# Performance work log

Hardware: AMD Instinct MI355X
Metric: run time of the kernel (lower is better)

The kernel has to match this reference:

```python
import jax, jax.numpy as jnp
import numpy as np

N = 100000   # nodes
E = 1600000  # edges (avg in-degree 16)
D = 128      # feature dim (in_feats == out_feats)


def setup_inputs() -> dict:
    key = jax.random.key(0)
    ks = jax.random.split(key, 8)
    h = jax.random.normal(ks[0], (N, D), dtype=jnp.float32)
    src = jax.random.randint(ks[1], (E,), 0, N)
    dst = jax.random.randint(ks[2], (E,), 0, N)
    # Xavier-uniform linear weights (gain ~ relu per reset_parameters)
    gain = float(np.sqrt(2.0))
    bound = gain * float(np.sqrt(6.0 / (D + D)))
    def w(k):
        return jax.random.uniform(k, (D, D), jnp.float32, -bound, bound)
    return {
        "h": h, "src": src, "dst": dst,
        "W_self0": w(ks[3]), "b_self0": jnp.zeros((D,), jnp.float32), "W_neigh0": w(ks[4]),
        "W_self1": w(ks[5]), "b_self1": jnp.zeros((D,), jnp.float32), "W_neigh1": w(ks[6]),
    }


def _sage_mean(x, src, dst, W_self, b_self, W_neigh):
    """DGL SAGEConv('mean') with in_feats == out_feats (lin_before_mp False):
    neigh = mean_{(u->v) in E} x[u]; out = fc_self(x) + fc_neigh(neigh)."""
    msg = x[src]  # [E, D] gather along edges
    ssum = jax.ops.segment_sum(msg, dst, num_segments=N)          # [N, D]
    deg = jax.ops.segment_sum(jnp.ones((src.shape[0],), x.dtype), dst, num_segments=N)
    neigh = jnp.where(deg[:, None] > 0, ssum / jnp.maximum(deg, 1.0)[:, None], 0.0)
    return x @ W_self.T + b_self + neigh @ W_neigh.T


def reference(h, src, dst, W_self0, b_self0, W_neigh0, W_self1, b_self1, W_neigh1):
    # SAGENet.forward (eval mode: no DropEdge, no feat dropout)
    t1 = _sage_mean(h, src, dst, W_self0, b_self0, W_neigh0)
    t2 = _sage_mean(t1, src, dst, W_self1, b_self1, W_neigh1)
    # res = sum over outs = [h, t1/1, t2/2]
    return h + t1 + t2 * 0.5
```

## Files before the change

### kernel.cpp

```cpp
#include <hip/hip_runtime.h>

#define D 128
#define NPC 128
#define NBUCKC 782
#define BCAPC 2560
#define NPB 32
#define BCAP 768
#define BIN_THREADS 512
#define BIN_CHUNK 8192

typedef __bf16 bf16x8 __attribute__((ext_vector_type(8)));
typedef __bf16 bf16x4 __attribute__((ext_vector_type(4)));
typedef float f32x4 __attribute__((ext_vector_type(4)));
typedef float f32x2 __attribute__((ext_vector_type(2)));

__global__ void k_wfrag(const float* __restrict__ A, const float* __restrict__ B,
                        const float* __restrict__ C2, const float* __restrict__ Dp,
                        __bf16* __restrict__ o) {
    int t = blockIdx.x * 256 + threadIdx.x;
    int m = t >> 11, r = t & 2047;
    int kb = r >> 9, nf = (r >> 6) & 7, l = r & 63;
    int lr = l & 15, lg = l >> 4;
    const float* W = (m == 0) ? A : (m == 1) ? B : (m == 2) ? C2 : Dp;
    const float* p = W + (nf * 16 + lr) * D + kb * 32 + lg * 8;
    bf16x8 v;
#pragma unroll
    for (int j = 0; j < 8; ++j) v[j] = (__bf16)p[j];
    *(bf16x8*)(o + (size_t)t * 8) = v;
}

__global__ void k_hconv(const float* __restrict__ x, __bf16* __restrict__ obf,
                        uint2* __restrict__ of8, int n8) {
    int i = blockIdx.x * 256 + threadIdx.x;
    if (i >= n8) return;
    const float4* x4 = (const float4*)x;
    float4 u = x4[(size_t)i * 2];
    float4 v = x4[(size_t)i * 2 + 1];
    bf16x8 r;
    r[0] = (__bf16)u.x; r[1] = (__bf16)u.y; r[2] = (__bf16)u.z; r[3] = (__bf16)u.w;
    r[4] = (__bf16)v.x; r[5] = (__bf16)v.y; r[6] = (__bf16)v.z; r[7] = (__bf16)v.w;
    *(bf16x8*)(obf + (size_t)i * 8) = r;
    int w0 = __builtin_amdgcn_cvt_pk_fp8_f32(u.x, u.y, 0, false);
    w0 = __builtin_amdgcn_cvt_pk_fp8_f32(u.z, u.w, w0, true);
    int w1 = __builtin_amdgcn_cvt_pk_fp8_f32(v.x, v.y, 0, false);
    w1 = __builtin_amdgcn_cvt_pk_fp8_f32(v.z, v.w, w1, true);
    of8[i] = make_uint2((unsigned)w0, (unsigned)w1);
}

__global__ void k_cvt8(const __bf16* __restrict__ x, uint2* __restrict__ of8, int n8) {
    int i = blockIdx.x * 256 + threadIdx.x;
    if (i >= n8) return;
    bf16x8 v = *(const bf16x8*)(x + (size_t)i * 8);
    int w0 = __builtin_amdgcn_cvt_pk_fp8_f32((float)v[0], (float)v[1], 0, false);
    w0 = __builtin_amdgcn_cvt_pk_fp8_f32((float)v[2], (float)v[3], w0, true);
    int w1 = __builtin_amdgcn_cvt_pk_fp8_f32((float)v[4], (float)v[5], 0, false);
    w1 = __builtin_amdgcn_cvt_pk_fp8_f32((float)v[6], (float)v[7], w1, true);
    of8[i] = make_uint2((unsigned)w0, (unsigned)w1);
}

__global__ __launch_bounds__(BIN_THREADS) void k_bin(
    const int* __restrict__ src, const int* __restrict__ dst,
    int* __restrict__ bcnt, unsigned int* __restrict__ bbuf, int E) {
    __shared__ int hist[NBUCKC];
    __shared__ int rbase[NBUCKC];
    __shared__ int lcur[NBUCKC];
    int tid = threadIdx.x;
    int e0 = blockIdx.x * BIN_CHUNK;
    int e1 = min(e0 + BIN_CHUNK, E);
    for (int i = tid; i < NBUCKC; i += BIN_THREADS) hist[i] = 0;
    __syncthreads();
    for (int i = e0 + tid; i < e1; i += BIN_THREADS)
        atomicAdd(&hist[dst[i] >> 7], 1);
    __syncthreads();
    for (int i = tid; i < NBUCKC; i += BIN_THREADS) {
        int c = hist[i];
        rbase[i] = (c > 0) ? atomicAdd(&bcnt[i], c) : 0;
        lcur[i] = 0;
    }
    __syncthreads();
    for (int i = e0 + tid; i < e1; i += BIN_THREADS) {
        int d = dst[i];
        int b = d >> 7;
        int pos = rbase[b] + atomicAdd(&lcur[b], 1);
        if (pos < BCAPC)
            bbuf[(size_t)b * BCAPC + pos] =
                ((unsigned)(d & 127) << 17) | (unsigned)src[i];
    }
}

__global__ __launch_bounds__(256) void k_bagg(
    const uint2* __restrict__ X8,
    const unsigned int* __restrict__ bbuf, const int* __restrict__ bcnt,
    __bf16* __restrict__ NEI, int n) {
    __shared__ int lnbr[BCAP];
    __shared__ int ldeg[NPB];
    __shared__ int lrow[NPB];
    __shared__ int lcur[NPB];
    int b = blockIdx.x;
    int tid = threadIdx.x;
    int cb = b >> 2;
    int sub = b & 3;
    int base = b * NPB;
    int nb = min(NPB, n - base);
    int cnt = min(bcnt[cb], BCAPC);
    const unsigned int* bb = bbuf + (size_t)cb * BCAPC;

    if (tid < NPB) { ldeg[tid] = 0; lcur[tid] = 0; }
    __syncthreads();
    for (int i = tid; i < cnt; i += 256) {
        int ld7 = (int)(bb[i] >> 17);
        if ((ld7 >> 5) == sub) atomicAdd(&ldeg[ld7 & 31], 1);
    }
    __syncthreads();
    if (tid < NPB) lrow[tid] = ldeg[tid];
    __syncthreads();
    for (int off = 1; off < NPB; off <<= 1) {
        int v = 0;
        if (tid < NPB && tid >= off) v = lrow[tid - off];
        __syncthreads();
        if (tid < NPB) lrow[tid] += v;
        __syncthreads();
    }
    for (int i = tid; i < cnt; i += 256) {
        unsigned e = bb[i];
        int ld7 = (int)(e >> 17);
        if ((ld7 >> 5) != sub) continue;
        int ld = ld7 & 31;
        int pos = (lrow[ld] - ldeg[ld]) + atomicAdd(&lcur[ld], 1);
        if (pos < BCAP) lnbr[pos] = (int)(e & 0x1FFFF);
    }
    __syncthreads();

    int slot = tid >> 4;
    int c = tid & 15;
#define DEC_ACC(w)                                                        \
    {                                                                     \
        f32x2 p0 = __builtin_amdgcn_cvt_pk_f32_fp8((w).x, false);         \
        f32x2 p1 = __builtin_amdgcn_cvt_pk_f32_fp8((w).x, true);          \
        f32x2 p2 = __builtin_amdgcn_cvt_pk_f32_fp8((w).y, false);         \
        f32x2 p3 = __builtin_amdgcn_cvt_pk_f32_fp8((w).y, true);          \
        a[0] += p0[0]; a[1] += p0[1]; a[2] += p1[0]; a[3] += p1[1];       \
        a[4] += p2[0]; a[5] += p2[1]; a[6] += p3[0]; a[7] += p3[1];       \
    }
#pragma unroll
    for (int it = 0; it < NPB / 16; ++it) {
        int node = it * 16 + slot;
        if (node >= nb) break;
        int dv = ldeg[node];
        int beg = lrow[node] - dv;
        float a[8];
#pragma unroll
        for (int j = 0; j < 8; ++j) a[j] = 0.f;
        int i = 0;
        for (; i + 7 < dv; i += 8) {
            uint2 w0 = X8[(size_t)lnbr[beg + i + 0] * 16 + c];
            uint2 w1 = X8[(size_t)lnbr[beg + i + 1] * 16 + c];
            uint2 w2 = X8[(size_t)lnbr[beg + i + 2] * 16 + c];
            uint2 w3 = X8[(size_t)lnbr[beg + i + 3] * 16 + c];
            uint2 w4 = X8[(size_t)lnbr[beg + i + 4] * 16 + c];
            uint2 w5 = X8[(size_t)lnbr[beg + i + 5] * 16 + c];
            uint2 w6 = X8[(size_t)lnbr[beg + i + 6] * 16 + c];
            uint2 w7 = X8[(size_t)lnbr[beg + i + 7] * 16 + c];
            DEC_ACC(w0) DEC_ACC(w1) DEC_ACC(w2) DEC_ACC(w3)
            DEC_ACC(w4) DEC_ACC(w5) DEC_ACC(w6) DEC_ACC(w7)
        }
        for (; i + 3 < dv; i += 4) {
            uint2 w0 = X8[(size_t)lnbr[beg + i + 0] * 16 + c];
            uint2 w1 = X8[(size_t)lnbr[beg + i + 1] * 16 + c];
            uint2 w2 = X8[(size_t)lnbr[beg + i + 2] * 16 + c];
            uint2 w3 = X8[(size_t)lnbr[beg + i + 3] * 16 + c];
            DEC_ACC(w0) DEC_ACC(w1) DEC_ACC(w2) DEC_ACC(w3)
        }
        for (; i < dv; ++i) {
            uint2 w0 = X8[(size_t)lnbr[beg + i] * 16 + c];
            DEC_ACC(w0)
        }
        float s = dv > 0 ? 1.0f / (float)dv : 0.0f;
        bf16x8 r;
#pragma unroll
        for (int j = 0; j < 8; ++j) r[j] = (__bf16)(a[j] * s);
        *(bf16x8*)(NEI + (size_t)(base + node) * D + c * 8) = r;
    }
#undef DEC_ACC
}

__global__ __launch_bounds__(256, 3) void k_gemm2(
    const __bf16* __restrict__ Xb, const __bf16* __restrict__ NEIb,
    const __bf16* __restrict__ Wfs, const __bf16* __restrict__ Wfn,
    const float* __restrict__ bs, const float* __restrict__ H,
    __bf16* __restrict__ t1out, float* __restrict__ out, int n, int final_mode) {
    __shared__ __bf16 wls[16384];

    int tid = threadIdx.x;
    int wave = tid >> 6;
    int lane = tid & 63;
    int lr = lane & 15;
    int lg = lane >> 4;
    int rowbase = blockIdx.x * 128 + wave * 32;

    bf16x8 xf[2][4];
#pragma unroll
    for (int mf = 0; mf < 2; ++mf) {
        int r = rowbase + mf * 16 + lr;
#pragma unroll
        for (int kb = 0; kb < 4; ++kb) {
            bf16x8 a = (bf16x8)(__bf16)0.f;
            if (r < n) a = *(const bf16x8*)(Xb + (size_t)r * D + kb * 32 + lg * 8);
            xf[mf][kb] = a;
        }
    }

    f32x4 acc[2][8];
#pragma unroll
    for (int mf = 0; mf < 2; ++mf)
#pragma unroll
        for (int nf = 0; nf < 8; ++nf) acc[mf][nf] = (f32x4)(0.f);

    {
        const bf16x8* s = (const bf16x8*)Wfs;
#pragma unroll
        for (int i = 0; i < 8; ++i) {
            bf16x8 v = s[i * 256 + tid];
            *(bf16x8*)(wls + (size_t)(i * 256 + tid) * 8) = v;
        }
    }
    __syncthreads();
#pragma unroll
    for (int kb = 0; kb < 4; ++kb) {
#pragma unroll
        for (int nf = 0; nf < 8; ++nf) {
            bf16x8 bfr = *(const bf16x8*)(wls + (size_t)((kb * 8 + nf) * 64 + lane) * 8);
            acc[0][nf] = __builtin_amdgcn_mfma_f32_16x16x32_bf16(xf[0][kb], bfr, acc[0][nf], 0, 0, 0);
            acc[1][nf] = __builtin_amdgcn_mfma_f32_16x16x32_bf16(xf[1][kb], bfr, acc[1][nf], 0, 0, 0);
        }
    }

    bf16x8 nfr[2][4];
#pragma unroll
    for (int mf = 0; mf < 2; ++mf) {
        int r = rowbase + mf * 16 + lr;
#pragma unroll
        for (int kb = 0; kb < 4; ++kb) {
            bf16x8 a = (bf16x8)(__bf16)0.f;
            if (r < n) a = *(const bf16x8*)(NEIb + (size_t)r * D + kb * 32 + lg * 8);
            nfr[mf][kb] = a;
        }
    }
    __syncthreads();
    {
        const bf16x8* s = (const bf16x8*)Wfn;
#pragma unroll
        for (int i = 0; i < 8; ++i) {
            bf16x8 v = s[i * 256 + tid];
            *(bf16x8*)(wls + (size_t)(i * 256 + tid) * 8) = v;
        }
    }
    __syncthreads();
#pragma unroll
    for (int kb = 0; kb < 4; ++kb) {
#pragma unroll
        for (int nf = 0; nf < 8; ++nf) {
            bf16x8 bfr = *(const bf16x8*)(wls + (size_t)((kb * 8 + nf) * 64 + lane) * 8);
            acc[0][nf] = __builtin_amdgcn_mfma_f32_16x16x32_bf16(nfr[0][kb], bfr, acc[0][nf], 0, 0, 0);
            acc[1][nf] = __builtin_amdgcn_mfma_f32_16x16x32_bf16(nfr[1][kb], bfr, acc[1][nf], 0, 0, 0);
        }
    }

#pragma unroll
    for (int mf = 0; mf < 2; ++mf) {
#pragma unroll
        for (int q = 0; q < 4; ++q) {
            int r = rowbase + mf * 16 + lg * 4 + q;
            if (r >= n) continue;
            if (final_mode) {
                const __bf16* t1p = Xb + (size_t)r * D;
#pragma unroll
                for (int nf = 0; nf < 8; ++nf) {
                    int j = nf * 16 + lr;
                    out[(size_t)r * D + j] =
                        H[(size_t)r * D + j] + (float)t1p[j] + 0.5f * (acc[mf][nf][q] + bs[j]);
                }
            } else {
                __bf16* dp = t1out + (size_t)r * D;
#pragma unroll
                for (int nf = 0; nf < 8; ++nf) {
                    int j = nf * 16 + lr;
                    dp[j] = (__bf16)(acc[mf][nf][q] + bs[j]);
                }
            }
        }
    }
}

extern "C" void kernel_launch(void* const* d_in, const int* in_sizes, int n_in,
                              void* d_out, int out_size, void* d_ws, size_t ws_size,
                              hipStream_t stream) {
    const float* h = (const float*)d_in[0];
    const int* src = (const int*)d_in[1];
    const int* dst = (const int*)d_in[2];
    const float* Ws0 = (const float*)d_in[3];
    const float* b0 = (const float*)d_in[4];
    const float* Wn0 = (const float*)d_in[5];
    const float* Ws1 = (const float*)d_in[6];
    const float* b1 = (const float*)d_in[7];
    const float* Wn1 = (const float*)d_in[8];
    float* out = (float*)d_out;

    int N = in_sizes[0] / D;
    int E = in_sizes[1];

    char* ws = (char*)d_ws;
    __bf16* hbf = (__bf16*)ws;   ws += (size_t)N * D * sizeof(__bf16);
    __bf16* t1b = (__bf16*)ws;   ws += (size_t)N * D * sizeof(__bf16);
    unsigned int* bbuf = (unsigned int*)ws; ws += (size_t)NBUCKC * BCAPC * sizeof(unsigned int);
    int* bcnt = (int*)ws;        ws += (size_t)NBUCKC * sizeof(int);
    __bf16* Wf = (__bf16*)ws;    ws += (size_t)4 * 2048 * 8 * sizeof(__bf16);
    __bf16* NEI1 = (__bf16*)d_out;
    uint2* F8 = (uint2*)((char*)d_out + ((size_t)32 << 20));
    __bf16* NEI2 = hbf;

    hipMemsetAsync(bcnt, 0, (size_t)NBUCKC * sizeof(int), stream);

    int n8 = N * D / 8;
    k_wfrag<<<32, 256, 0, stream>>>(Ws0, Wn0, Ws1, Wn1, Wf);
    k_hconv<<<(n8 + 255) / 256, 256, 0, stream>>>(h, hbf, F8, n8);
    k_bin<<<(E + BIN_CHUNK - 1) / BIN_CHUNK, BIN_THREADS, 0, stream>>>(src, dst, bcnt, bbuf, E);

    int gb = (N + 127) / 128;
    int ab = (N + NPB - 1) / NPB;
    k_bagg<<<ab, 256, 0, stream>>>(F8, bbuf, bcnt, NEI1, N);
    k_gemm2<<<gb, 256, 0, stream>>>(hbf, NEI1, Wf + 0 * 16384, Wf + 1 * 16384,
                                    b0, nullptr, t1b, nullptr, N, 0);
    k_cvt8<<<(n8 + 255) / 256, 256, 0, stream>>>(t1b, F8, n8);
    k_bagg<<<ab, 256, 0, stream>>>(F8, bbuf, bcnt, NEI2, N);
    k_gemm2<<<gb, 256, 0, stream>>>(t1b, NEI2, Wf + 2 * 16384, Wf + 3 * 16384,
                                    b1, h, nullptr, out, N, 1);
}
```

Before: 189.5 us.

## Fuse neighbor aggregation with dense GEMM into one per-layer kernel

Merges the aggregation kernel and the GEMM kernel into a single k_layer kernel. Mean-aggregated neighbor features stay in shared memory, and each 32-node block runs the self and neighbor MFMAs directly instead of writing and re-reading an NEI buffer. The layer-1 epilogue also writes the FP8 copy of t1, which removes the separate bf16 copy of h and the k_cvt8 pass. The cost is a smaller GEMM tile per block, loading the full weight matrices into LDS once per 32 rows instead of once per 128, and higher LDS use per block that may lower occupancy. It also drops the node-count bound check and leaves a dead load loop in the code.

```diff
diff --git a/kernel.cpp b/kernel.cpp
--- a/kernel.cpp
+++ b/kernel.cpp
@@ -1,16 +1,15 @@
 #include <hip/hip_runtime.h>
 
 #define D 128
-#define NPC 128
 #define NBUCKC 782
 #define BCAPC 2560
 #define NPB 32
 #define BCAP 768
 #define BIN_THREADS 512
 #define BIN_CHUNK 8192
+#define NEIW 140
 
 typedef __bf16 bf16x8 __attribute__((ext_vector_type(8)));
-typedef __bf16 bf16x4 __attribute__((ext_vector_type(4)));
 typedef float f32x4 __attribute__((ext_vector_type(4)));
 typedef float f32x2 __attribute__((ext_vector_type(2)));
 
@@ -29,32 +28,16 @@
     *(bf16x8*)(o + (size_t)t * 8) = v;
 }
 
-__global__ void k_hconv(const float* __restrict__ x, __bf16* __restrict__ obf,
-                        uint2* __restrict__ of8, int n8) {
+__global__ void k_hconv8(const float* __restrict__ x, uint2* __restrict__ of8, int n8) {
     int i = blockIdx.x * 256 + threadIdx.x;
     if (i >= n8) return;
     const float4* x4 = (const float4*)x;
     float4 u = x4[(size_t)i * 2];
     float4 v = x4[(size_t)i * 2 + 1];
-    bf16x8 r;
-    r[0] = (__bf16)u.x; r[1] = (__bf16)u.y; r[2] = (__bf16)u.z; r[3] = (__bf16)u.w;
-    r[4] = (__bf16)v.x; r[5] = (__bf16)v.y; r[6] = (__bf16)v.z; r[7] = (__bf16)v.w;
-    *(bf16x8*)(obf + (size_t)i * 8) = r;
     int w0 = __builtin_amdgcn_cvt_pk_fp8_f32(u.x, u.y, 0, false);
     w0 = __builtin_amdgcn_cvt_pk_fp8_f32(u.z, u.w, w0, true);
     int w1 = __builtin_amdgcn_cvt_pk_fp8_f32(v.x, v.y, 0, false);
     w1 = __builtin_amdgcn_cvt_pk_fp8_f32(v.z, v.w, w1, true);
-    of8[i] = make_uint2((unsigned)w0, (unsigned)w1);
-}
-
-__global__ void k_cvt8(const __bf16* __restrict__ x, uint2* __restrict__ of8, int n8) {
-    int i = blockIdx.x * 256 + threadIdx.x;
-    if (i >= n8) return;
-    bf16x8 v = *(const bf16x8*)(x + (size_t)i * 8);
-    int w0 = __builtin_amdgcn_cvt_pk_fp8_f32((float)v[0], (float)v[1], 0, false);
-    w0 = __builtin_amdgcn_cvt_pk_fp8_f32((float)v[2], (float)v[3], w0, true);
-    int w1 = __builtin_amdgcn_cvt_pk_fp8_f32((float)v[4], (float)v[5], 0, false);
-    w1 = __builtin_amdgcn_cvt_pk_fp8_f32((float)v[6], (float)v[7], w1, true);
     of8[i] = make_uint2((unsigned)w0, (unsigned)w1);
 }
 
@@ -88,22 +71,62 @@
     }
 }
 
-__global__ __launch_bounds__(256) void k_bagg(
+__global__ __launch_bounds__(256) void k_layer(
+    const float* __restrict__ Hf, const __bf16* __restrict__ T1,
     const uint2* __restrict__ X8,
     const unsigned int* __restrict__ bbuf, const int* __restrict__ bcnt,
-    __bf16* __restrict__ NEI, int n) {
+    const __bf16* __restrict__ Wfs, const __bf16* __restrict__ Wfn,
+    const float* __restrict__ bs,
+    __bf16* __restrict__ t1out, unsigned char* __restrict__ f8out,
+    float* __restrict__ out, int n, int final_mode) {
     __shared__ int lnbr[BCAP];
     __shared__ int ldeg[NPB];
     __shared__ int lrow[NPB];
     __shared__ int lcur[NPB];
+    __shared__ __bf16 nei[NPB * NEIW];
+    __shared__ __bf16 wls[16384];
+
     int b = blockIdx.x;
     int tid = threadIdx.x;
     int cb = b >> 2;
     int sub = b & 3;
     int base = b * NPB;
-    int nb = min(NPB, n - base);
     int cnt = min(bcnt[cb], BCAPC);
     const unsigned int* bb = bbuf + (size_t)cb * BCAPC;
+
+    int wave = tid >> 6;
+    int lane = tid & 63;
+    int lr = lane & 15;
+    int lg = lane >> 4;
+    int mf = wave & 1;
+    int nfh = wave >> 1;
+
+    bf16x8 xf[4];
+    {
+        int r = base + mf * 16 + lr;
+        if (final_mode) {
+#pragma unroll
+            for (int kb = 0; kb < 4; ++kb)
+                xf[kb] = *(const bf16x8*)(T1 + (size_t)r * D + kb * 32 + lg * 8);
+        } else {
+            const float4* p = (const float4*)(Hf + (size_t)r * D);
+#pragma unroll
+            for (int kb = 0; kb < 4; ++kb) {
+                float4 u = p[kb * 2 + (lg >> 1) * ((lg & 1) * 0)];
+                (void)u;
+            }
+#pragma unroll
+            for (int kb = 0; kb < 4; ++kb) {
+                const float4* q = (const float4*)(Hf + (size_t)r * D + kb * 32 + lg * 8);
+                float4 u = q[0];
+                float4 v = q[1];
+                bf16x8 a;
+                a[0] = (__bf16)u.x; a[1] = (__bf16)u.y; a[2] = (__bf16)u.z; a[3] = (__bf16)u.w;
+                a[4] = (__bf16)v.x; a[5] = (__bf16)v.y; a[6] = (__bf16)v.z; a[7] = (__bf16)v.w;
+                xf[kb] = a;
+            }
+        }
+    }
 
     if (tid < NPB) { ldeg[tid] = 0; lcur[tid] = 0; }
     __syncthreads();
@@ -131,26 +154,30 @@
     }
     __syncthreads();
 
+    {
+        const bf16x8* s = (const bf16x8*)Wfs;
+#pragma unroll
+        for (int i = 0; i < 8; ++i) {
+            bf16x8 v = s[i * 256 + tid];
+            *(bf16x8*)(wls + (size_t)(i * 256 + tid) * 8) = v;
+        }
+    }
+
     int slot = tid >> 4;
     int c = tid & 15;
 #define DEC_ACC(w)                                                        \
     {                                                                     \
-        f32x2 p0 = __builtin_amdgcn_cvt_pk_f32_fp8((w).x, false);         \
-        f32x2 p1 = __builtin_amdgcn_cvt_pk_f32_fp8((w).x, true);          \
-        f32x2 p2 = __builtin_amdgcn_cvt_pk_f32_fp8((w).y, false);         \
-        f32x2 p3 = __builtin_amdgcn_cvt_pk_f32_fp8((w).y, true);          \
-        a[0] += p0[0]; a[1] += p0[1]; a[2] += p1[0]; a[3] += p1[1];       \
-        a[4] += p2[0]; a[5] += p2[1]; a[6] += p3[0]; a[7] += p3[1];       \
+        a0 += __builtin_amdgcn_cvt_pk_f32_fp8((w).x, false);              \
+        a1 += __builtin_amdgcn_cvt_pk_f32_fp8((w).x, true);               \
+        a2 += __builtin_amdgcn_cvt_pk_f32_fp8((w).y, false);              \
+        a3 += __builtin_amdgcn_cvt_pk_f32_fp8((w).y, true);               \
     }
 #pragma unroll
     for (int it = 0; it < NPB / 16; ++it) {
         int node = it * 16 + slot;
-        if (node >= nb) break;
         int dv = ldeg[node];
         int beg = lrow[node] - dv;
-        float a[8];
-#pragma unroll
-        for (int j = 0; j < 8; ++j) a[j] = 0.f;
+        f32x2 a0 = (f32x2)(0.f), a1 = (f32x2)(0.f), a2 = (f32x2)(0.f), a3 = (f32x2)(0.f);
         int i = 0;
         for (; i + 7 < dv; i += 8) {
             uint2 w0 = X8[(size_t)lnbr[beg + i + 0] * 16 + c];
@@ -177,47 +204,30 @@
         }
         float s = dv > 0 ? 1.0f / (float)dv : 0.0f;
         bf16x8 r;
-#pragma unroll
-        for (int j = 0; j < 8; ++j) r[j] = (__bf16)(a[j] * s);
-        *(bf16x8*)(NEI + (size_t)(base + node) * D + c * 8) = r;
+        r[0] = (__bf16)(a0[0] * s); r[1] = (__bf16)(a0[1] * s);
+        r[2] = (__bf16)(a1[0] * s); r[3] = (__bf16)(a1[1] * s);
+        r[4] = (__bf16)(a2[0] * s); r[5] = (__bf16)(a2[1] * s);
+        r[6] = (__bf16)(a3[0] * s); r[7] = (__bf16)(a3[1] * s);
+        *(bf16x8*)(nei + node * NEIW + c * 8) = r;
     }
 #undef DEC_ACC
-}
-
-__global__ __launch_bounds__(256, 3) void k_gemm2(
-    const __bf16* __restrict__ Xb, const __bf16* __restrict__ NEIb,
-    const __bf16* __restrict__ Wfs, const __bf16* __restrict__ Wfn,
-    const float* __restrict__ bs, const float* __restrict__ H,
-    __bf16* __restrict__ t1out, float* __restrict__ out, int n, int final_mode) {
-    __shared__ __bf16 wls[16384];
-
-    int tid = threadIdx.x;
-    int wave = tid >> 6;
-    int lane = tid & 63;
-    int lr = lane & 15;
-    int lg = lane >> 4;
-    int rowbase = blockIdx.x * 128 + wave * 32;
-
-    bf16x8 xf[2][4];
-#pragma unroll
-    for (int mf = 0; mf < 2; ++mf) {
-        int r = rowbase + mf * 16 + lr;
-#pragma unroll
-        for (int kb = 0; kb < 4; ++kb) {
-            bf16x8 a = (bf16x8)(__bf16)0.f;
-            if (r < n) a = *(const bf16x8*)(Xb + (size_t)r * D + kb * 32 + lg * 8);
-            xf[mf][kb] = a;
-        }
-    }
-
-    f32x4 acc[2][8];
-#pragma unroll
-    for (int mf = 0; mf < 2; ++mf)
-#pragma unroll
-        for (int nf = 0; nf < 8; ++nf) acc[mf][nf] = (f32x4)(0.f);
-
+    __syncthreads();
+
+    f32x4 acc[4];
+#pragma unroll
+    for (int nfl = 0; nfl < 4; ++nfl) acc[nfl] = (f32x4)(0.f);
+#pragma unroll
+    for (int kb = 0; kb < 4; ++kb) {
+#pragma unroll
+        for (int nfl = 0; nfl < 4; ++nfl) {
+            int nf = nfh * 4 + nfl;
+            bf16x8 bfr = *(const bf16x8*)(wls + (size_t)((kb * 8 + nf) * 64 + lane) * 8);
+            acc[nfl] = __builtin_amdgcn_mfma_f32_16x16x32_bf16(xf[kb], bfr, acc[nfl], 0, 0, 0);
+        }
+    }
+    __syncthreads();
     {
-        const bf16x8* s = (const bf16x8*)Wfs;
+        const bf16x8* s = (const bf16x8*)Wfn;
 #pragma unroll
         for (int i = 0; i < 8; ++i) {
             bf16x8 v = s[i * 256 + tid];
@@ -227,66 +237,36 @@
     __syncthreads();
 #pragma unroll
     for (int kb = 0; kb < 4; ++kb) {
-#pragma unroll
-        for (int nf = 0; nf < 8; ++nf) {
+        bf16x8 af = *(const bf16x8*)(nei + (mf * 16 + lr) * NEIW + kb * 32 + lg * 8);
+#pragma unroll
+        for (int nfl = 0; nfl < 4; ++nfl) {
+            int nf = nfh * 4 + nfl;
             bf16x8 bfr = *(const bf16x8*)(wls + (size_t)((kb * 8 + nf) * 64 + lane) * 8);
-            acc[0][nf] = __builtin_amdgcn_mfma_f32_16x16x32_bf16(xf[0][kb], bfr, acc[0][nf], 0, 0, 0);
-            acc[1][nf] = __builtin_amdgcn_mfma_f32_16x16x32_bf16(xf[1][kb], bfr, acc[1][nf], 0, 0, 0);
-        }
-    }
-
-    bf16x8 nfr[2][4];
-#pragma unroll
-    for (int mf = 0; mf < 2; ++mf) {
-        int r = rowbase + mf * 16 + lr;
-#pragma unroll
-        for (int kb = 0; kb < 4; ++kb) {
-            bf16x8 a = (bf16x8)(__bf16)0.f;
-            if (r < n) a = *(const bf16x8*)(NEIb + (size_t)r * D + kb * 32 + lg * 8);
-            nfr[mf][kb] = a;
-        }
-    }
-    __syncthreads();
-    {
-        const bf16x8* s = (const bf16x8*)Wfn;
-#pragma unroll
-        for (int i = 0; i < 8; ++i) {
-            bf16x8 v = s[i * 256 + tid];
-            *(bf16x8*)(wls + (size_t)(i * 256 + tid) * 8) = v;
-        }
-    }
-    __syncthreads();
-#pragma unroll
-    for (int kb = 0; kb < 4; ++kb) {
-#pragma unroll
-        for (int nf = 0; nf < 8; ++nf) {
-            bf16x8 bfr = *(const bf16x8*)(wls + (size_t)((kb * 8 + nf) * 64 + lane) * 8);
-            acc[0][nf] = __builtin_amdgcn_mfma_f32_16x16x32_bf16(nfr[0][kb], bfr, acc[0][nf], 0, 0, 0);
-            acc[1][nf] = __builtin_amdgcn_mfma_f32_16x16x32_bf16(nfr[1][kb], bfr, acc[1][nf], 0, 0, 0);
-        }
-    }
-
-#pragma unroll
-    for (int mf = 0; mf < 2; ++mf) {
-#pragma unroll
-        for (int q = 0; q < 4; ++q) {
-            int r = rowbase + mf * 16 + lg * 4 + q;
-            if (r >= n) continue;
-            if (final_mode) {
-                const __bf16* t1p = Xb + (size_t)r * D;
-#pragma unroll
-                for (int nf = 0; nf < 8; ++nf) {
-                    int j = nf * 16 + lr;
-                    out[(size_t)r * D + j] =
-                        H[(size_t)r * D + j] + (float)t1p[j] + 0.5f * (acc[mf][nf][q] + bs[j]);
-                }
-            } else {
-                __bf16* dp = t1out + (size_t)r * D;
-#pragma unroll
-                for (int nf = 0; nf < 8; ++nf) {
-                    int j = nf * 16 + lr;
-                    dp[j] = (__bf16)(acc[mf][nf][q] + bs[j]);
-                }
+            acc[nfl] = __builtin_amdgcn_mfma_f32_16x16x32_bf16(af, bfr, acc[nfl], 0, 0, 0);
+        }
+    }
+
+#pragma unroll
+    for (int q = 0; q < 4; ++q) {
+        int r = base + mf * 16 + lg * 4 + q;
+        if (r >= n) continue;
+        if (final_mode) {
+#pragma unroll
+            for (int nfl = 0; nfl < 4; ++nfl) {
+                int j = (nfh * 4 + nfl) * 16 + lr;
+                out[(size_t)r * D + j] = Hf[(size_t)r * D + j] + (float)T1[(size_t)r * D + j]
+                                         + 0.5f * (acc[nfl][q] + bs[j]);
+            }
+        } else {
+            __bf16* dp = t1out + (size_t)r * D;
+            unsigned char* fp = f8out + (size_t)r * D;
+#pragma unroll
+            for (int nfl = 0; nfl < 4; ++nfl) {
+                int j = (nfh * 4 + nfl) * 16 + lr;
+                float t = acc[nfl][q] + bs[j];
+                dp[j] = (__bf16)t;
+                int w8 = __builtin_amdgcn_cvt_pk_fp8_f32(t, t, 0, false);
+                fp[j] = (unsigned char)(w8 & 0xff);
             }
         }
     }
@@ -310,29 +290,25 @@
     int E = in_sizes[1];
 
     char* ws = (char*)d_ws;
-    __bf16* hbf = (__bf16*)ws;   ws += (size_t)N * D * sizeof(__bf16);
     __bf16* t1b = (__bf16*)ws;   ws += (size_t)N * D * sizeof(__bf16);
-    unsigned int* bbuf = (unsigned int*)ws; ws += (size_t)NBUCKC * BCAPC * sizeof(unsigned int);
+    unsigned int* bbuf = (unsigned int*)ws; ws += (size_t)NBUCKC * BCAPC * 4;
     int* bcnt = (int*)ws;        ws += (size_t)NBUCKC * sizeof(int);
     __bf16* Wf = (__bf16*)ws;    ws += (size_t)4 * 2048 * 8 * sizeof(__bf16);
-    __bf16* NEI1 = (__bf16*)d_out;
-    uint2* F8 = (uint2*)((char*)d_out + ((size_t)32 << 20));
-    __bf16* NEI2 = hbf;
+    uint2* F8t1 = (uint2*)ws;    ws += (size_t)N * D;
+    uint2* F8h = (uint2*)((char*)d_out + ((size_t)32 << 20));
 
     hipMemsetAsync(bcnt, 0, (size_t)NBUCKC * sizeof(int), stream);
 
     int n8 = N * D / 8;
     k_wfrag<<<32, 256, 0, stream>>>(Ws0, Wn0, Ws1, Wn1, Wf);
-    k_hconv<<<(n8 + 255) / 256, 256, 0, stream>>>(h, hbf, F8, n8);
+    k_hconv8<<<(n8 + 255) / 256, 256, 0, stream>>>(h, F8h, n8);
     k_bin<<<(E + BIN_CHUNK - 1) / BIN_CHUNK, BIN_THREADS, 0, stream>>>(src, dst, bcnt, bbuf, E);
 
-    int gb = (N + 127) / 128;
-    int ab = (N + NPB - 1) / NPB;
-    k_bagg<<<ab, 256, 0, stream>>>(F8, bbuf, bcnt, NEI1, N);
-    k_gemm2<<<gb, 256, 0, stream>>>(hbf, NEI1, Wf + 0 * 16384, Wf + 1 * 16384,
-                                    b0, nullptr, t1b, nullptr, N, 0);
-    k_cvt8<<<(n8 + 255) / 256, 256, 0, stream>>>(t1b, F8, n8);
-    k_bagg<<<ab, 256, 0, stream>>>(F8, bbuf, bcnt, NEI2, N);
-    k_gemm2<<<gb, 256, 0, stream>>>(t1b, NEI2, Wf + 2 * 16384, Wf + 3 * 16384,
-                                    b1, h, nullptr, out, N, 1);
-}
+    int lb = (N + NPB - 1) / NPB;
+    k_layer<<<lb, 256, 0, stream>>>(h, t1b, F8h, bbuf, bcnt,
+                                    Wf + 0 * 16384, Wf + 1 * 16384, b0,
+                                    t1b, (unsigned char*)F8t1, nullptr, N, 0);
+    k_layer<<<lb, 256, 0, stream>>>(h, t1b, F8t1, bbuf, bcnt,
+                                    Wf + 2 * 16384, Wf + 3 * 16384, b1,
+                                    nullptr, nullptr, out, N, 1);
+}
```

Result: slower. 232.0 us (+22.4%).
